# Optimization experiments

Hardware: AMD Instinct MI355X
Metric: run time of the kernel (lower is better)

The kernel has to match this reference:

```python
import jax, jax.numpy as jnp
import numpy as np

D_MODEL = 512
N_HEADS = 8
HEAD_DIM = D_MODEL // N_HEADS
D_FF = 2048
RADIUS = 1                      # manhattan_radius
MAX_LEVEL = 2                   # layer_max_level
WINDOWS = (512, 64, 16)         # window_size_per_level


def _layer_norm(x, g, b, eps=1e-5):
    mu = jnp.mean(x, axis=-1, keepdims=True)
    var = jnp.mean(jnp.square(x - mu), axis=-1, keepdims=True)
    return (x - mu) * jax.lax.rsqrt(var + eps) * g + b


def setup_inputs() -> dict:
    key = jax.random.key(0)
    ks = jax.random.split(key, 16)
    B, N = 2, 2048
    s = 0.02
    return {
        "x": jax.random.normal(ks[0], (B, N, D_MODEL), jnp.float32),
        "coords_pos": jax.random.randint(ks[1], (B, N, 2), 0, 64, jnp.int32),
        "coords_level": jax.random.randint(ks[2], (B, N), 0, 3, jnp.int32),
        "w_qkv": jax.random.normal(ks[3], (D_MODEL, 3 * D_MODEL), jnp.float32) * s,
        "b_qkv": jnp.zeros((3 * D_MODEL,), jnp.float32),
        "w_out": jax.random.normal(ks[4], (D_MODEL, D_MODEL), jnp.float32) * s,
        "b_out": jnp.zeros((D_MODEL,), jnp.float32),
        "w_ff1": jax.random.normal(ks[5], (D_MODEL, D_FF), jnp.float32) * s,
        "b_ff1": jnp.zeros((D_FF,), jnp.float32),
        "w_ff2": jax.random.normal(ks[6], (D_FF, D_MODEL), jnp.float32) * s,
        "b_ff2": jnp.zeros((D_MODEL,), jnp.float32),
        "ln1_g": jnp.ones((D_MODEL,), jnp.float32),
        "ln1_b": jnp.zeros((D_MODEL,), jnp.float32),
        "ln2_g": jnp.ones((D_MODEL,), jnp.float32),
        "ln2_b": jnp.zeros((D_MODEL,), jnp.float32),
    }


def _geometric_mask(coords_pos, coords_level):
    """[B,N,N] bool mask: same hierarchy level, Manhattan distance <= RADIUS,
    within the per-level sequence window, levels <= MAX_LEVEL; self always allowed."""
    B, N = coords_level.shape
    # Manhattan distance on grid coords  [B,N,N]
    dist = jnp.sum(jnp.abs(coords_pos[:, :, None, :] - coords_pos[:, None, :, :]), axis=-1)
    same_level = coords_level[:, :, None] == coords_level[:, None, :]
    lvl_ok = coords_level <= MAX_LEVEL                       # [B,N]
    lvl_pair = lvl_ok[:, :, None] & lvl_ok[:, None, :]
    win_tab = jnp.array(WINDOWS, jnp.int32)
    win_q = win_tab[jnp.clip(coords_level, 0, len(WINDOWS) - 1)]  # [B,N]
    idx = jnp.arange(N, dtype=jnp.int32)
    seq_dist = jnp.abs(idx[:, None] - idx[None, :])          # [N,N]
    in_window = seq_dist[None] < win_q[:, :, None]
    eye = jnp.eye(N, dtype=bool)[None]
    return (same_level & (dist <= RADIUS) & in_window & lvl_pair) | eye


def reference(x, coords_pos, coords_level, w_qkv, b_qkv, w_out, b_out,
              w_ff1, b_ff1, w_ff2, b_ff2, ln1_g, ln1_b, ln2_g, ln2_b):
    B, N, D = x.shape
    residual = x
    xn = _layer_norm(x, ln1_g, ln1_b)
    qkv = (xn @ w_qkv + b_qkv).reshape(B, N, 3, N_HEADS, HEAD_DIM)
    q, k, v = qkv[:, :, 0], qkv[:, :, 1], qkv[:, :, 2]        # [B,N,H,Dh]

    scale = 1.0 / np.sqrt(HEAD_DIM)
    scores = jnp.einsum("bihd,bjhd->bhij", q, k) * scale      # [B,H,N,N]
    mask = _geometric_mask(coords_pos, coords_level)          # [B,N,N]
    scores = jnp.where(mask[:, None], scores, jnp.float32(-1e9))
    probs = jax.nn.softmax(scores, axis=-1)
    attn = jnp.einsum("bhij,bjhd->bihd", probs, v).reshape(B, N, D)
    x = residual + (attn @ w_out + b_out)                     # dropout = identity (eval)

    residual = x
    xn = _layer_norm(x, ln2_g, ln2_b)
    h = jax.nn.gelu(xn @ w_ff1 + b_ff1, approximate=False)
    x = residual + (h @ w_ff2 + b_ff2)
    return x
```

## Files before the change

### kernel.cpp

```cpp
#include <hip/hip_runtime.h>
#include <hip/hip_bf16.h>

#define DMODEL 512
#define NHEADS 8
#define DFF 2048
#define NSEQ 2048
#define NROWS 4096

typedef __attribute__((ext_vector_type(8))) short   bf16x8;
typedef __attribute__((ext_vector_type(4))) float   f32x4;
typedef __attribute__((ext_vector_type(8))) unsigned short u16x8;

__device__ __forceinline__ unsigned short f2bf(float f) {
  union { float f; unsigned u; } v; v.f = f;
  unsigned r = v.u + 0x7fffu + ((v.u >> 16) & 1u);
  return (unsigned short)(r >> 16);
}
__device__ __forceinline__ float bf2f(unsigned short u) {
  union { unsigned u; float f; } v; v.u = (unsigned)u << 16;
  return v.f;
}

#define GLL16(src, dst) \
  __builtin_amdgcn_global_load_lds((__attribute__((address_space(1))) const void*)(src), \
                                   (__attribute__((address_space(3))) void*)(dst), 16, 0, 0)

__global__ __launch_bounds__(256)
void prep(const float* __restrict__ w_qkv, const float* __restrict__ w_out,
          const float* __restrict__ w_ff1, const float* __restrict__ w_ff2,
          const float* __restrict__ ln1_g, const float* __restrict__ ln1_b,
          const float* __restrict__ ln2_g, const float* __restrict__ ln2_b,
          const float* __restrict__ b_qkv, const float* __restrict__ b_ff1,
          const float* __restrict__ x,
          unsigned short* __restrict__ wqkvT, unsigned short* __restrict__ woutT,
          unsigned short* __restrict__ wff1T, unsigned short* __restrict__ wff2T,
          float* __restrict__ vq, float* __restrict__ uq,
          float* __restrict__ vf, float* __restrict__ uf,
          unsigned short* __restrict__ x_bf, float2* __restrict__ stats1,
          float* __restrict__ stats2) {
  __shared__ char smem_raw[12288];
  int bid = blockIdx.x;
  const int tid = threadIdx.x;
  if (bid < 3072) {
    unsigned short (*t)[33] = (unsigned short (*)[33])smem_raw;
    const float* w; unsigned short* wT; const float* g; int K, N;
    if (bid < 768)       { w = w_qkv; wT = wqkvT; g = ln1_g; K = 512;  N = 1536; }
    else if (bid < 1024) { bid -= 768;  w = w_out; wT = woutT; g = nullptr; K = 512;  N = 512; }
    else if (bid < 2048) { bid -= 1024; w = w_ff1; wT = wff1T; g = ln2_g; K = 512;  N = 2048; }
    else                 { bid -= 2048; w = w_ff2; wT = wff2T; g = nullptr; K = 2048; N = 512; }
    const int ntx = N >> 5;
    const int n0 = (bid % ntx) * 32, k0 = (bid / ntx) * 32;
    const int tx = tid & 31, ty = tid >> 5;
    #pragma unroll
    for (int i = 0; i < 4; ++i) {
      const int k = k0 + ty + i * 8;
      const float s = g ? g[k] : 1.0f;
      t[ty + i * 8][tx] = f2bf(s * w[(size_t)k * N + n0 + tx]);
    }
    __syncthreads();
    #pragma unroll
    for (int i = 0; i < 4; ++i)
      wT[(size_t)(n0 + ty + i * 8) * K + k0 + tx] = t[tx][ty + i * 8];
  } else if (bid < 3100) {
    const int b = bid - 3072;
    const float *w, *g, *bb, *bias; float *ov, *ou; int N, n0;
    if (b < 12) { w = w_qkv; g = ln1_g; bb = ln1_b; bias = b_qkv;
                  ov = vq; ou = uq; N = 1536; n0 = b * 128; }
    else        { w = w_ff1; g = ln2_g; bb = ln2_b; bias = b_ff1;
                  ov = vf; ou = uf; N = 2048; n0 = (b - 12) * 128; }
    float*  sg = (float*)smem_raw;
    float*  sb = sg + 512;
    float4* pu = (float4*)(sb + 512);
    float4* pv = pu + 256;
    sg[tid] = g[tid];  sg[tid + 256] = g[tid + 256];
    sb[tid] = bb[tid]; sb[tid + 256] = bb[tid + 256];
    __syncthreads();
    const int c4 = tid & 31, kg = tid >> 5;
    float4 su = make_float4(0, 0, 0, 0), sv = make_float4(0, 0, 0, 0);
    const float* wp = w + (size_t)(kg * 64) * N + n0 + c4 * 4;
    #pragma unroll 8
    for (int kk = 0; kk < 64; ++kk) {
      const float4 wv = *(const float4*)(wp + (size_t)kk * N);
      const float gk = sg[kg * 64 + kk], bk = sb[kg * 64 + kk];
      su.x = fmaf(bk, wv.x, su.x); su.y = fmaf(bk, wv.y, su.y);
      su.z = fmaf(bk, wv.z, su.z); su.w = fmaf(bk, wv.w, su.w);
      sv.x = fmaf(gk, wv.x, sv.x); sv.y = fmaf(gk, wv.y, sv.y);
      sv.z = fmaf(gk, wv.z, sv.z); sv.w = fmaf(gk, wv.w, sv.w);
    }
    pu[kg * 32 + c4] = su; pv[kg * 32 + c4] = sv;
    __syncthreads();
    if (tid < 32) {
      float4 u = pu[tid], v = pv[tid];
      #pragma unroll
      for (int q = 1; q < 8; ++q) {
        const float4 a = pu[q * 32 + tid], c = pv[q * 32 + tid];
        u.x += a.x; u.y += a.y; u.z += a.z; u.w += a.w;
        v.x += c.x; v.y += c.y; v.z += c.z; v.w += c.w;
      }
      const float4 bv = *(const float4*)(bias + n0 + tid * 4);
      u.x += bv.x; u.y += bv.y; u.z += bv.z; u.w += bv.w;
      *(float4*)(ov + n0 + tid * 4) = v;
      *(float4*)(ou + n0 + tid * 4) = u;
    }
  } else if (bid < 4124) {
    const int row = (bid - 3100) * 4 + (tid >> 6);
    const int lane = tid & 63;
    const float* xr = x + (size_t)row * DMODEL + lane * 8;
    const float4 v0 = *(const float4*)(xr);
    const float4 v1 = *(const float4*)(xr + 4);
    float s  = v0.x + v0.y + v0.z + v0.w + v1.x + v1.y + v1.z + v1.w;
    float s2 = v0.x*v0.x + v0.y*v0.y + v0.z*v0.z + v0.w*v0.w
             + v1.x*v1.x + v1.y*v1.y + v1.z*v1.z + v1.w*v1.w;
    #pragma unroll
    for (int m = 1; m < 64; m <<= 1) {
      s  += __shfl_xor(s,  m);
      s2 += __shfl_xor(s2, m);
    }
    const float mu  = s * (1.0f / DMODEL);
    const float var = s2 * (1.0f / DMODEL) - mu * mu;
    const float rs  = rsqrtf(var + 1e-5f);
    if (lane == 0) stats1[row] = make_float2(mu, rs);
    u16x8 o;
    o[0] = f2bf(v0.x); o[1] = f2bf(v0.y); o[2] = f2bf(v0.z); o[3] = f2bf(v0.w);
    o[4] = f2bf(v1.x); o[5] = f2bf(v1.y); o[6] = f2bf(v1.z); o[7] = f2bf(v1.w);
    *(u16x8*)(x_bf + (size_t)row * DMODEL + lane * 8) = o;
  } else {
    const int idx = (bid - 4124) * 256 + tid;
    if (idx < 2 * NROWS) stats2[idx] = 0.0f;
  }
}

template<int MODE, int BM>
__global__ __launch_bounds__(256)
void gemm_bf16(const unsigned short* __restrict__ A,
               const unsigned short* __restrict__ Bt,
               const float* __restrict__ bias,
               const float* __restrict__ v, const float* __restrict__ u,
               const float* __restrict__ resf, const unsigned short* __restrict__ resb,
               float* __restrict__ stats, void* __restrict__ Cout,
               int M, int N, int LDA, int KL) {
  constexpr int MR = BM / 32;
  constexpr int PS = BM / 32 + 2;
  constexpr int ROWS = BM / 2;
  __shared__ unsigned short As[3][BM * 64];
  __shared__ unsigned short Bs[3][64 * 64];

  const int tid = threadIdx.x;
  const int w = tid >> 6, l = tid & 63;
  const int gx = N >> 6;
  const int nxy = gx * (M / BM);
  int lin = blockIdx.x;
  lin = (lin & 7) * (nxy >> 3) + (lin >> 3);
  const int bn = (lin % gx) << 6;
  const int bm = (lin / gx) * BM;
  const int wr = (w >> 1) * (BM >> 1);
  const int wc = (w & 1) * 32;
  const int lr = l & 15, kg = l >> 4;

  f32x4 acc[MR][2] = {};

  auto stage = [&](int buf, int k0) {
    #pragma unroll
    for (int i = 0; i < BM / 32; ++i) {
      const int g = i * 4 + w;
      const int c = g * 64 + l;
      const int row = c >> 3;
      const int kc = (c & 7) ^ (row & 7);
      GLL16(A + (size_t)(bm + row) * LDA + k0 + kc * 8, &As[buf][g * 512]);
    }
    #pragma unroll
    for (int i = 0; i < 2; ++i) {
      const int g = i * 4 + w;
      const int c = g * 64 + l;
      const int row = c >> 3;
      const int kc = (c & 7) ^ (row & 7);
      GLL16(Bt + (size_t)(bn + row) * LDA + k0 + kc * 8, &Bs[buf][g * 512]);
    }
  };

  const int nt = KL >> 6;
  stage(0, 0);
  stage(1, 64);
  for (int t = 0; t < nt; ++t) {
    if (t + 1 < nt) {
      asm volatile("s_waitcnt vmcnt(%0)" :: "n"(PS) : "memory");
    } else {
      asm volatile("s_waitcnt vmcnt(0)" ::: "memory");
    }
    __builtin_amdgcn_sched_barrier(0);
    __builtin_amdgcn_s_barrier();
    __builtin_amdgcn_sched_barrier(0);
    if (t + 2 < nt) stage((t + 2) % 3, (t + 2) << 6);
    const int cur = t % 3;
    #pragma unroll
    for (int ks = 0; ks < 2; ++ks) {
      const int cc = ks * 4 + kg;
      bf16x8 af[MR], bfv[2];
      #pragma unroll
      for (int mi = 0; mi < MR; ++mi) {
        const int row = wr + mi * 16 + lr;
        af[mi] = *(const bf16x8*)&As[cur][(row * 8 + (cc ^ (row & 7))) * 8];
      }
      #pragma unroll
      for (int ni = 0; ni < 2; ++ni) {
        const int row = wc + ni * 16 + lr;
        bfv[ni] = *(const bf16x8*)&Bs[cur][(row * 8 + (cc ^ (row & 7))) * 8];
      }
      __builtin_amdgcn_s_setprio(1);
      #pragma unroll
      for (int mi = 0; mi < MR; ++mi)
        #pragma unroll
        for (int ni = 0; ni < 2; ++ni)
          acc[mi][ni] = __builtin_amdgcn_mfma_f32_16x16x32_bf16(
              af[mi], bfv[ni], acc[mi][ni], 0, 0, 0);
      __builtin_amdgcn_s_setprio(0);
    }
  }

  __syncthreads();
  float* sc = ((float*)&As[0][0]) + w * (ROWS * 36);
  #pragma unroll
  for (int mi = 0; mi < MR; ++mi)
    #pragma unroll
    for (int ni = 0; ni < 2; ++ni)
      #pragma unroll
      for (int reg = 0; reg < 4; ++reg)
        sc[(mi * 16 + kg * 4 + reg) * 36 + ni * 16 + lr] = acc[mi][ni][reg];

  float* Cf = (float*)Cout;
  unsigned short* Cb = (unsigned short*)Cout;
  const int r2 = l >> 2, ch = l & 3;
  #pragma unroll
  for (int i2 = 0; i2 < ROWS / 16; ++i2) {
    const int rl = i2 * 16 + r2;
    const int grow = bm + wr + rl;
    const int c0 = ch * 8;
    const int gcol = bn + wc + c0;
    const float4 va = *(const float4*)&sc[rl * 36 + c0];
    const float4 vb = *(const float4*)&sc[rl * 36 + c0 + 4];
    float vals[8] = {va.x, va.y, va.z, va.w, vb.x, vb.y, vb.z, vb.w};

    if (MODE == 4 || MODE == 6) {
      float mu, rs;
      if (MODE == 4) {
        const float2 st = ((const float2*)stats)[grow];
        mu = st.x; rs = st.y;
      } else {
        const float2 st = ((const float2*)stats)[grow];
        mu = st.x * (1.0f / DMODEL);
        rs = rsqrtf(st.y * (1.0f / DMODEL) - mu * mu + 1e-5f);
      }
      const float4 v0 = *(const float4*)&v[gcol];
      const float4 v1 = *(const float4*)&v[gcol + 4];
      const float4 u0 = *(const float4*)&u[gcol];
      const float4 u1 = *(const float4*)&u[gcol + 4];
      const float vv[8] = {v0.x, v0.y, v0.z, v0.w, v1.x, v1.y, v1.z, v1.w};
      const float uu[8] = {u0.x, u0.y, u0.z, u0.w, u1.x, u1.y, u1.z, u1.w};
      #pragma unroll
      for (int e = 0; e < 8; ++e) {
        float t = rs * (vals[e] - mu * vv[e]) + uu[e];
        if (MODE == 6) t = 0.5f * t * (1.0f + erff(t * 0.70710678118654752f));
        vals[e] = t;
      }
      u16x8 o;
      #pragma unroll
      for (int e = 0; e < 8; ++e) o[e] = f2bf(vals[e]);
      *(u16x8*)&Cb[(size_t)grow * N + gcol] = o;
    }

    if (MODE == 5) {
      const float4 b0 = *(const float4*)&bias[gcol];
      const float4 b1 = *(const float4*)&bias[gcol + 4];
      const float4 r0 = *(const float4*)&resf[(size_t)grow * N + gcol];
      const float4 r1 = *(const float4*)&resf[(size_t)grow * N + gcol + 4];
      const float bb[8] = {b0.x, b0.y, b0.z, b0.w, b1.x, b1.y, b1.z, b1.w};
      const float rr[8] = {r0.x, r0.y, r0.z, r0.w, r1.x, r1.y, r1.z, r1.w};
      float rsum = 0.0f, rsq = 0.0f;
      u16x8 o;
      #pragma unroll
      for (int e = 0; e < 8; ++e) {
        const float t = vals[e] + bb[e] + rr[e];
        o[e] = f2bf(t);
        rsum += t; rsq = fmaf(t, t, rsq);
      }
      *(u16x8*)&Cb[(size_t)grow * N + gcol] = o;
      rsum += __shfl_xor(rsum, 1); rsq += __shfl_xor(rsq, 1);
      rsum += __shfl_xor(rsum, 2); rsq += __shfl_xor(rsq, 2);
      if (ch == 0) {
        atomicAdd(&stats[2 * grow],     rsum);
        atomicAdd(&stats[2 * grow + 1], rsq);
      }
    }

    if (MODE == 7) {
      const float4 b0 = *(const float4*)&bias[gcol];
      const float4 b1 = *(const float4*)&bias[gcol + 4];
      const u16x8 rb = *(const u16x8*)&resb[(size_t)grow * N + gcol];
      const float bb[8] = {b0.x, b0.y, b0.z, b0.w, b1.x, b1.y, b1.z, b1.w};
      #pragma unroll
      for (int e = 0; e < 8; ++e) vals[e] += bb[e] + bf2f(rb[e]);
      *(float4*)&Cf[(size_t)grow * N + gcol] =
          make_float4(vals[0], vals[1], vals[2], vals[3]);
      *(float4*)&Cf[(size_t)grow * N + gcol + 4] =
          make_float4(vals[4], vals[5], vals[6], vals[7]);
    }
  }
}

#define CAP 256
__global__ __launch_bounds__(64)
void attn_kernel(const unsigned short* __restrict__ qkv,
                 const int* __restrict__ pos, const int* __restrict__ lvl,
                 unsigned short* __restrict__ out) {
  const int r = blockIdx.x;
  const int i = r & (NSEQ - 1);
  const int base = r - i;
  const int lane = threadIdx.x;

  __shared__ int   s_idx[CAP];
  __shared__ int   s_cnt;
  __shared__ float s_sc[NHEADS][CAP];
  __shared__ float s_inv[NHEADS];

  if (lane == 0) s_cnt = 0;
  __syncthreads();

  const int li = lvl[r];
  const int2 pq = *(const int2*)(pos + 2 * r);
  const int win = (li == 0) ? 512 : (li == 1 ? 64 : 16);
  const int jlo = max(i - win + 1, 0);
  const int jhi = min(i + win - 1, NSEQ - 1);

  for (int j = jlo + lane; j <= jhi; j += 64) {
    const int rj = base + j;
    bool m = (j == i);
    if (!m) {
      const int lj = lvl[rj];
      const int2 pj = *(const int2*)(pos + 2 * rj);
      const int d = abs(pq.x - pj.x) + abs(pq.y - pj.y);
      m = (lj == li) && (d <= 1);
    }
    if (m) {
      const int p = atomicAdd(&s_cnt, 1);
      if (p < CAP) s_idx[p] = j;
    }
  }
  __syncthreads();
  const int cnt = min(s_cnt, CAP);

  const u16x8 qv = *(const u16x8*)(qkv + (size_t)r * 1536 + lane * 8);
  float qf[8];
  #pragma unroll
  for (int e = 0; e < 8; ++e) qf[e] = bf2f(qv[e]);

  for (int jj = 0; jj < cnt; ++jj) {
    const int rj = base + s_idx[jj];
    const u16x8 kv = *(const u16x8*)(qkv + (size_t)rj * 1536 + 512 + lane * 8);
    float p = 0.0f;
    #pragma unroll
    for (int e = 0; e < 8; ++e) p = fmaf(qf[e], bf2f(kv[e]), p);
    p += __shfl_xor(p, 1);
    p += __shfl_xor(p, 2);
    p += __shfl_xor(p, 4);
    if ((lane & 7) == 0) s_sc[lane >> 3][jj] = p * 0.125f;
  }
  __syncthreads();

  if (lane < 8) {
    float mx = -1e30f;
    for (int jj = 0; jj < cnt; ++jj) mx = fmaxf(mx, s_sc[lane][jj]);
    float den = 0.0f;
    for (int jj = 0; jj < cnt; ++jj) {
      const float e = expf(s_sc[lane][jj] - mx);
      s_sc[lane][jj] = e;
      den += e;
    }
    s_inv[lane] = 1.0f / den;
  }
  __syncthreads();

  const int h = lane >> 3;
  float a[8] = {};
  for (int jj = 0; jj < cnt; ++jj) {
    const float pp = s_sc[h][jj];
    const u16x8 vv = *(const u16x8*)(qkv + (size_t)(base + s_idx[jj]) * 1536 + 1024 + lane * 8);
    #pragma unroll
    for (int e = 0; e < 8; ++e) a[e] = fmaf(pp, bf2f(vv[e]), a[e]);
  }
  const float inv = s_inv[h];
  u16x8 o;
  #pragma unroll
  for (int e = 0; e < 8; ++e) o[e] = f2bf(a[e] * inv);
  *(u16x8*)(out + (size_t)r * DMODEL + lane * 8) = o;
}

extern "C" void kernel_launch(void* const* d_in, const int* in_sizes, int n_in,
                              void* d_out, int out_size, void* d_ws, size_t ws_size,
                              hipStream_t stream) {
  const float* x            = (const float*)d_in[0];
  const int*   coords_pos   = (const int*)d_in[1];
  const int*   coords_level = (const int*)d_in[2];
  const float* w_qkv        = (const float*)d_in[3];
  const float* b_qkv        = (const float*)d_in[4];
  const float* w_out        = (const float*)d_in[5];
  const float* b_out        = (const float*)d_in[6];
  const float* w_ff1        = (const float*)d_in[7];
  const float* b_ff1        = (const float*)d_in[8];
  const float* w_ff2        = (const float*)d_in[9];
  const float* b_ff2        = (const float*)d_in[10];
  const float* ln1_g        = (const float*)d_in[11];
  const float* ln1_b        = (const float*)d_in[12];
  const float* ln2_g        = (const float*)d_in[13];
  const float* ln2_b        = (const float*)d_in[14];
  float* out = (float*)d_out;

  char* ws = (char*)d_ws;
  unsigned short* qkv_bf = (unsigned short*)(ws);
  unsigned short* h_bf   = (unsigned short*)(ws);
  unsigned short* x_bf   = (unsigned short*)(ws + 16777216);
  unsigned short* at_bf  = (unsigned short*)(ws + 20971520);
  unsigned short* x1_bf  = (unsigned short*)(ws + 25165824);
  unsigned short* wqkvT  = (unsigned short*)(ws + 29360128);
  unsigned short* woutT  = (unsigned short*)(ws + 30932992);
  unsigned short* wff1T  = (unsigned short*)(ws + 31457280);
  unsigned short* wff2T  = (unsigned short*)(ws + 33554432);
  float*          vq     = (float*)(ws + 35651584);
  float*          uq     = (float*)(ws + 35657728);
  float*          vf     = (float*)(ws + 35663872);
  float*          uf     = (float*)(ws + 35672064);
  float2*         stats1 = (float2*)(ws + 35680256);
  float*          stats2 = (float*)(ws + 35713024);

  prep<<<4156, 256, 0, stream>>>(w_qkv, w_out, w_ff1, w_ff2,
                                 ln1_g, ln1_b, ln2_g, ln2_b, b_qkv, b_ff1, x,
                                 wqkvT, woutT, wff1T, wff2T,
                                 vq, uq, vf, uf, x_bf, stats1, stats2);

  gemm_bf16<4, 128><<<(1536/64)*(NROWS/128), 256, 0, stream>>>(
      x_bf, wqkvT, nullptr, vq, uq, nullptr, nullptr, (float*)stats1,
      qkv_bf, NROWS, 1536, DMODEL, DMODEL);

  attn_kernel<<<NROWS, 64, 0, stream>>>(qkv_bf, coords_pos, coords_level, at_bf);

  gemm_bf16<5, 64><<<(DMODEL/64)*(NROWS/64), 256, 0, stream>>>(
      at_bf, woutT, b_out, nullptr, nullptr, x, nullptr, stats2,
      x1_bf, NROWS, DMODEL, DMODEL, DMODEL);

  gemm_bf16<6, 128><<<(DFF/64)*(NROWS/128), 256, 0, stream>>>(
      x1_bf, wff1T, nullptr, vf, uf, nullptr, nullptr, stats2,
      h_bf, NROWS, DFF, DMODEL, DMODEL);

  gemm_bf16<7, 64><<<(DMODEL/64)*(NROWS/64), 256, 0, stream>>>(
      h_bf, wff2T, b_ff2, nullptr, nullptr, nullptr, x1_bf, nullptr,
      out, NROWS, DMODEL, DFF, DFF);
}
```

Before: 99.41 us.

## Add 128x128-tile GEMM kernel for QKV and FF1 projections

Adds a dedicated gemm128 kernel with 128x128 output tiles, 4x4 MFMA fragments per wave and double-buffered LDS, used for the QKV and FF1 GEMMs whose epilogues apply LayerNorm (and GELU for FF1). The LayerNorm epilogue is removed from the generic kernel, which keeps only the residual modes. Larger tiles raise arithmetic intensity and halve B-tile reloads, at the cost of fewer blocks (384 and 512), more registers and less stage depth (2 instead of 3 buffers).

```diff
diff --git a/kernel.cpp b/kernel.cpp
--- a/kernel.cpp
+++ b/kernel.cpp
@@ -130,12 +130,137 @@
   }
 }
 
+template<int MODE>
+__global__ __launch_bounds__(256)
+void gemm128(const unsigned short* __restrict__ A,
+             const unsigned short* __restrict__ Bt,
+             const float* __restrict__ v, const float* __restrict__ u,
+             const float* __restrict__ stats, unsigned short* __restrict__ Cb,
+             int M, int N, int LDA, int KL) {
+  __shared__ unsigned short As[2][128 * 64];
+  __shared__ unsigned short Bs[2][128 * 64];
+
+  const int tid = threadIdx.x;
+  const int w = tid >> 6, l = tid & 63;
+  const int gx = N >> 7;
+  const int nxy = gx * (M >> 7);
+  int lin = blockIdx.x;
+  lin = (lin & 7) * (nxy >> 3) + (lin >> 3);
+  const int bn = (lin % gx) << 7;
+  const int bm = (lin / gx) << 7;
+  const int wr = (w >> 1) * 64;
+  const int wc = (w & 1) * 64;
+  const int lr = l & 15, kg = l >> 4;
+
+  f32x4 acc[4][4] = {};
+
+  auto stage = [&](int buf, int k0) {
+    #pragma unroll
+    for (int i = 0; i < 4; ++i) {
+      const int g = i * 4 + w;
+      const int c = g * 64 + l;
+      const int row = c >> 3;
+      const int kc = (c & 7) ^ (row & 7);
+      GLL16(A + (size_t)(bm + row) * LDA + k0 + kc * 8, &As[buf][g * 512]);
+    }
+    #pragma unroll
+    for (int i = 0; i < 4; ++i) {
+      const int g = i * 4 + w;
+      const int c = g * 64 + l;
+      const int row = c >> 3;
+      const int kc = (c & 7) ^ (row & 7);
+      GLL16(Bt + (size_t)(bn + row) * LDA + k0 + kc * 8, &Bs[buf][g * 512]);
+    }
+  };
+
+  const int nt = KL >> 6;
+  stage(0, 0);
+  for (int t = 0; t < nt; ++t) {
+    asm volatile("s_waitcnt vmcnt(0)" ::: "memory");
+    __builtin_amdgcn_sched_barrier(0);
+    __builtin_amdgcn_s_barrier();
+    __builtin_amdgcn_sched_barrier(0);
+    if (t + 1 < nt) stage((t + 1) & 1, (t + 1) << 6);
+    const int cur = t & 1;
+    #pragma unroll
+    for (int ks = 0; ks < 2; ++ks) {
+      const int cc = ks * 4 + kg;
+      bf16x8 af[4], bfv[4];
+      #pragma unroll
+      for (int mi = 0; mi < 4; ++mi) {
+        const int row = wr + mi * 16 + lr;
+        af[mi] = *(const bf16x8*)&As[cur][(row * 8 + (cc ^ (row & 7))) * 8];
+      }
+      #pragma unroll
+      for (int ni = 0; ni < 4; ++ni) {
+        const int row = wc + ni * 16 + lr;
+        bfv[ni] = *(const bf16x8*)&Bs[cur][(row * 8 + (cc ^ (row & 7))) * 8];
+      }
+      __builtin_amdgcn_s_setprio(1);
+      #pragma unroll
+      for (int mi = 0; mi < 4; ++mi)
+        #pragma unroll
+        for (int ni = 0; ni < 4; ++ni)
+          acc[mi][ni] = __builtin_amdgcn_mfma_f32_16x16x32_bf16(
+              af[mi], bfv[ni], acc[mi][ni], 0, 0, 0);
+      __builtin_amdgcn_s_setprio(0);
+    }
+    __builtin_amdgcn_s_barrier();
+  }
+
+  __syncthreads();
+  float* sc = ((float*)&As[0][0]) + w * (64 * 36);
+  const int r2 = l >> 2, ch = l & 3, c0 = ch * 8;
+  #pragma unroll
+  for (int p = 0; p < 2; ++p) {
+    #pragma unroll
+    for (int mi = 0; mi < 4; ++mi)
+      #pragma unroll
+      for (int ni = 0; ni < 2; ++ni)
+        #pragma unroll
+        for (int reg = 0; reg < 4; ++reg)
+          sc[(mi * 16 + kg * 4 + reg) * 36 + ni * 16 + lr] = acc[mi][p * 2 + ni][reg];
+    #pragma unroll
+    for (int i2 = 0; i2 < 4; ++i2) {
+      const int rl = i2 * 16 + r2;
+      const int grow = bm + wr + rl;
+      const int gcol = bn + wc + p * 32 + c0;
+      const float4 va = *(const float4*)&sc[rl * 36 + c0];
+      const float4 vb = *(const float4*)&sc[rl * 36 + c0 + 4];
+      float vals[8] = {va.x, va.y, va.z, va.w, vb.x, vb.y, vb.z, vb.w};
+      float mu, rs;
+      if (MODE == 4) {
+        const float2 st = ((const float2*)stats)[grow];
+        mu = st.x; rs = st.y;
+      } else {
+        const float2 st = ((const float2*)stats)[grow];
+        mu = st.x * (1.0f / DMODEL);
+        rs = rsqrtf(st.y * (1.0f / DMODEL) - mu * mu + 1e-5f);
+      }
+      const float4 v0 = *(const float4*)&v[gcol];
+      const float4 v1 = *(const float4*)&v[gcol + 4];
+      const float4 u0 = *(const float4*)&u[gcol];
+      const float4 u1 = *(const float4*)&u[gcol + 4];
+      const float vv[8] = {v0.x, v0.y, v0.z, v0.w, v1.x, v1.y, v1.z, v1.w};
+      const float uu[8] = {u0.x, u0.y, u0.z, u0.w, u1.x, u1.y, u1.z, u1.w};
+      u16x8 o;
+      #pragma unroll
+      for (int e = 0; e < 8; ++e) {
+        float t = rs * (vals[e] - mu * vv[e]) + uu[e];
+        if (MODE == 6) t = 0.5f * t * (1.0f + erff(t * 0.70710678118654752f));
+        o[e] = f2bf(t);
+      }
+      *(u16x8*)&Cb[(size_t)grow * N + gcol] = o;
+    }
+    if (p == 0) __builtin_amdgcn_s_barrier();
+  }
+}
+
 template<int MODE, int BM>
 __global__ __launch_bounds__(256)
 void gemm_bf16(const unsigned short* __restrict__ A,
                const unsigned short* __restrict__ Bt,
                const float* __restrict__ bias,
-               const float* __restrict__ v, const float* __restrict__ u,
                const float* __restrict__ resf, const unsigned short* __restrict__ resb,
                float* __restrict__ stats, void* __restrict__ Cout,
                int M, int N, int LDA, int KL) {
@@ -239,34 +364,6 @@
     const float4 va = *(const float4*)&sc[rl * 36 + c0];
     const float4 vb = *(const float4*)&sc[rl * 36 + c0 + 4];
     float vals[8] = {va.x, va.y, va.z, va.w, vb.x, vb.y, vb.z, vb.w};
-
-    if (MODE == 4 || MODE == 6) {
-      float mu, rs;
-      if (MODE == 4) {
-        const float2 st = ((const float2*)stats)[grow];
-        mu = st.x; rs = st.y;
-      } else {
-        const float2 st = ((const float2*)stats)[grow];
-        mu = st.x * (1.0f / DMODEL);
-        rs = rsqrtf(st.y * (1.0f / DMODEL) - mu * mu + 1e-5f);
-      }
-      const float4 v0 = *(const float4*)&v[gcol];
-      const float4 v1 = *(const float4*)&v[gcol + 4];
-      const float4 u0 = *(const float4*)&u[gcol];
-      const float4 u1 = *(const float4*)&u[gcol + 4];
-      const float vv[8] = {v0.x, v0.y, v0.z, v0.w, v1.x, v1.y, v1.z, v1.w};
-      const float uu[8] = {u0.x, u0.y, u0.z, u0.w, u1.x, u1.y, u1.z, u1.w};
-      #pragma unroll
-      for (int e = 0; e < 8; ++e) {
-        float t = rs * (vals[e] - mu * vv[e]) + uu[e];
-        if (MODE == 6) t = 0.5f * t * (1.0f + erff(t * 0.70710678118654752f));
-        vals[e] = t;
-      }
-      u16x8 o;
-      #pragma unroll
-      for (int e = 0; e < 8; ++e) o[e] = f2bf(vals[e]);
-      *(u16x8*)&Cb[(size_t)grow * N + gcol] = o;
-    }
 
     if (MODE == 5) {
       const float4 b0 = *(const float4*)&bias[gcol];
@@ -436,21 +533,17 @@
                                  wqkvT, woutT, wff1T, wff2T,
                                  vq, uq, vf, uf, x_bf, stats1, stats2);
 
-  gemm_bf16<4, 128><<<(1536/64)*(NROWS/128), 256, 0, stream>>>(
-      x_bf, wqkvT, nullptr, vq, uq, nullptr, nullptr, (float*)stats1,
-      qkv_bf, NROWS, 1536, DMODEL, DMODEL);
+  gemm128<4><<<(1536/128)*(NROWS/128), 256, 0, stream>>>(
+      x_bf, wqkvT, vq, uq, (const float*)stats1, qkv_bf, NROWS, 1536, DMODEL, DMODEL);
 
   attn_kernel<<<NROWS, 64, 0, stream>>>(qkv_bf, coords_pos, coords_level, at_bf);
 
   gemm_bf16<5, 64><<<(DMODEL/64)*(NROWS/64), 256, 0, stream>>>(
-      at_bf, woutT, b_out, nullptr, nullptr, x, nullptr, stats2,
-      x1_bf, NROWS, DMODEL, DMODEL, DMODEL);
-
-  gemm_bf16<6, 128><<<(DFF/64)*(NROWS/128), 256, 0, stream>>>(
-      x1_bf, wff1T, nullptr, vf, uf, nullptr, nullptr, stats2,
-      h_bf, NROWS, DFF, DMODEL, DMODEL);
+      at_bf, woutT, b_out, x, nullptr, stats2, x1_bf, NROWS, DMODEL, DMODEL, DMODEL);
+
+  gemm128<6><<<(DFF/128)*(NROWS/128), 256, 0, stream>>>(
+      x1_bf, wff1T, vf, uf, stats2, h_bf, NROWS, DFF, DMODEL, DMODEL);
 
   gemm_bf16<7, 64><<<(DMODEL/64)*(NROWS/64), 256, 0, stream>>>(
-      h_bf, wff2T, b_ff2, nullptr, nullptr, nullptr, x1_bf, nullptr,
-      out, NROWS, DMODEL, DFF, DFF);
-}
+      h_bf, wff2T, b_ff2, nullptr, x1_bf, nullptr, out, NROWS, DMODEL, DFF, DFF);
+}
```

After: 92.48 us. 7.0% less time.
